# Optimization experiments

Measured on AMD Instinct MI355X. Metric: run time of the kernel, lower is better.

## Reference

```python
import jax, jax.numpy as jnp
import numpy as np

K = 0.001  # sigmoid temperature from DGCLoss init
EPS = 1e-8


def _off_diag(m):
    # [..., n, n] -> [..., n, n-1], removing the diagonal in row-major order
    n = m.shape[-1]
    lead = m.shape[:-2]
    flat = m.reshape(lead + (n * n,))[..., :-1]
    return flat.reshape(lead + (n - 1, n + 1))[..., 1:].reshape(lead + (n, n - 1))


def setup_inputs() -> dict:
    key = jax.random.key(0)
    k1, k2 = jax.random.split(key)
    ranking = jax.random.normal(k1, (384, 256), dtype=jnp.float32)
    gt = jax.random.randint(k2, (384,), 0, 6, dtype=jnp.int64)
    return {"ranking": ranking, "gt": gt}


def reference(ranking, gt):
    x = ranking
    N = x.shape[0]
    # cosine similarity matrix, mapped to [0, 1]
    xn = x / jnp.clip(jnp.linalg.norm(x, axis=1, keepdims=True), EPS, None)
    sm = (xn @ xn.T + 1.0) * 0.5                         # [N, N]
    rank = _off_diag(sm)                                 # [N, N-1]
    g = jnp.abs(gt[None, :] - gt[:, None]).astype(jnp.float32)  # [N, N]
    g = _off_diag(g)                                     # [N, N-1]
    M = N - 1
    # dij[n, i, j] = rank[n, j] - rank[n, i]
    dij = rank[:, None, :] - rank[:, :, None]            # [N, M, M]
    dij = _off_diag(dij)                                 # [N, M, M-1]
    # clamped sigmoid indicator
    indicator = 1.0 / (1.0 + jnp.exp(jnp.clip(-dij / K, -50.0, 50.0)))
    indicator = indicator.sum(-1) + 1.0                  # [N, M]
    relevance = jnp.exp2(jnp.clip(10.0 - g, 0.0, None)) - 1.0  # [N, M]
    dcg = (relevance / jnp.log2(indicator + 1.0)).sum(axis=1)  # [N]
    # ideal DCG from sorted relevance
    rel_sorted = jnp.sort(relevance, axis=-1)[:, ::-1]
    discount = jnp.log2(jnp.arange(M, dtype=jnp.float32) + 2.0)
    idcg = (rel_sorted / discount).sum(axis=-1)          # [N]
    valid = idcg != 0.0
    ndcg = jnp.where(valid, dcg / jnp.where(valid, idcg, 1.0), 0.0)
    cnt = valid.sum()
    mean_ndcg = ndcg.sum() / jnp.maximum(cnt, 1).astype(jnp.float32)
    return jnp.where(cnt == 0, jnp.float32(1.0), 1.0 - mean_ndcg)
```

## Files before the change

### kernel.cpp

```cpp
#include <hip/hip_runtime.h>


#define NN 384
#define DD 256
#define MM 383
#define HSCALE 721.3475204444817f
#define NBUCK  256
#define BSCALE 0.1767955801104972f
#define WWIN   16.0f

__global__ __launch_bounds__(256) void dgc_normT(const float* __restrict__ x,
                                                 float* __restrict__ XT,
                                                 float* __restrict__ XN,
                                                 float* __restrict__ out) {
    __shared__ float xs[16][260];
    __shared__ float invn[16];

    const int t  = threadIdx.x;
    const int r0 = blockIdx.x * 16;

    if (blockIdx.x == 0 && t == 0) out[0] = 1.0f;

    #pragma unroll
    for (int i = 0; i < 4; ++i) {
        int f = t + i * 256;
        int r = f >> 6, c4 = f & 63;
        float4 v = ((const float4*)(x + (size_t)(r0 + r) * DD))[c4];
        xs[r][c4 * 4 + 0] = v.x; xs[r][c4 * 4 + 1] = v.y;
        xs[r][c4 * 4 + 2] = v.z; xs[r][c4 * 4 + 3] = v.w;
    }
    __syncthreads();

    {
        const int r = t >> 4, sub = t & 15;
        float s = 0.0f;
        #pragma unroll
        for (int m = 0; m < 16; ++m) {
            float v = xs[r][sub * 16 + m];
            s = fmaf(v, v, s);
        }
        #pragma unroll
        for (int off = 8; off > 0; off >>= 1) s += __shfl_xor(s, off, 64);
        if (sub == 0) invn[r] = __builtin_amdgcn_rsqf(fmaxf(s, 1e-16f));
    }
    __syncthreads();

    {
        const int r  = t & 15;
        const int kk = t >> 4;
        const float inv = invn[r];
        #pragma unroll
        for (int i = 0; i < 16; ++i) {
            int k = i * 16 + kk;
            XT[(size_t)k * NN + r0 + r] = xs[r][k] * inv;
        }
    }
    {
        #pragma unroll
        for (int i = 0; i < 4; ++i) {
            int f = t + i * 256;
            int r = f >> 6, c4 = f & 63;
            const float inv = invn[r];
            float4 v;
            v.x = xs[r][c4 * 4 + 0] * inv; v.y = xs[r][c4 * 4 + 1] * inv;
            v.z = xs[r][c4 * 4 + 2] * inv; v.w = xs[r][c4 * 4 + 3] * inv;
            ((float4*)(XN + (size_t)(r0 + r) * DD))[c4] = v;
        }
    }
}

__global__ __launch_bounds__(384) void dgc_gram(const float* __restrict__ XN,
                                                const float* __restrict__ XT,
                                                float* __restrict__ S) {
    __shared__ __align__(16) float xs4[DD][4];

    const int t  = threadIdx.x;
    const int n0 = blockIdx.x * 4;

    if (t < 256) {
        int r = t >> 6, c4 = t & 63;
        float4 v = ((const float4*)(XN + (size_t)(n0 + r) * DD))[c4];
        xs4[c4 * 4 + 0][r] = v.x; xs4[c4 * 4 + 1][r] = v.y;
        xs4[c4 * 4 + 2][r] = v.z; xs4[c4 * 4 + 3][r] = v.w;
    }
    __syncthreads();

    const int j = t;
    float a0 = 0.f, a1 = 0.f, a2 = 0.f, a3 = 0.f;
    #pragma unroll 8
    for (int k = 0; k < DD; ++k) {
        float b = XT[(size_t)k * NN + j];
        float4 s = *(const float4*)xs4[k];
        a0 = fmaf(s.x, b, a0); a1 = fmaf(s.y, b, a1);
        a2 = fmaf(s.z, b, a2); a3 = fmaf(s.w, b, a3);
    }
    S[(size_t)(n0 + 0) * NN + j] = fmaf(a0, HSCALE, HSCALE);
    S[(size_t)(n0 + 1) * NN + j] = fmaf(a1, HSCALE, HSCALE);
    S[(size_t)(n0 + 2) * NN + j] = fmaf(a2, HSCALE, HSCALE);
    S[(size_t)(n0 + 3) * NN + j] = fmaf(a3, HSCALE, HSCALE);
}

__global__ __launch_bounds__(384) void dgc_body(const float* __restrict__ S,
                                                const int* __restrict__ gt,
                                                float* __restrict__ out) {
    __shared__ float vsort[NN];
    __shared__ int   sidx[NN];
    __shared__ int   hist[NBUCK];
    __shared__ int   pre[NBUCK + 1];
    __shared__ float sn_sh;
    __shared__ float redd[6], redi[6];
    __shared__ int   ghist[6], gcum[6];

    const int n    = blockIdx.x;
    const int t    = threadIdx.x;
    const int lane = t & 63;
    const int wave = t >> 6;

    const float vraw = S[(size_t)n * NN + t];
    if (t < NBUCK) hist[t] = 0;
    if (t < 6) ghist[t] = 0;
    if (t == n) sn_sh = vraw;
    __syncthreads();

    int b = (int)(vraw * BSCALE);
    b = b < 0 ? 0 : (b > NBUCK - 1 ? NBUCK - 1 : b);
    const int slot = atomicAdd(&hist[b], 1);
    __syncthreads();

    if (wave == 0) {
        const int s0 = hist[lane * 4 + 0], s1 = hist[lane * 4 + 1];
        const int s2 = hist[lane * 4 + 2], s3 = hist[lane * 4 + 3];
        const int sum = s0 + s1 + s2 + s3;
        int inc = sum;
        #pragma unroll
        for (int off = 1; off < 64; off <<= 1) {
            int u = __shfl_up(inc, off, 64);
            if (lane >= off) inc += u;
        }
        const int base = inc - sum;
        pre[lane * 4 + 0] = base;
        pre[lane * 4 + 1] = base + s0;
        pre[lane * 4 + 2] = base + s0 + s1;
        pre[lane * 4 + 3] = base + s0 + s1 + s2;
        if (lane == 63) pre[NBUCK] = inc;
    }
    __syncthreads();

    {
        const int pos = pre[b] + slot;
        vsort[pos] = vraw;
        sidx[pos]  = t;
    }
    __syncthreads();

    const float ri    = vsort[t];
    const int   iorig = sidx[t];
    const float sn    = sn_sh;

    int Blo = (int)((ri - WWIN) * BSCALE);
    int Bhi = (int)((ri + WWIN) * BSCALE);
    Blo = Blo < 0 ? 0 : (Blo > NBUCK - 1 ? NBUCK - 1 : Blo);
    Bhi = Bhi < 0 ? 0 : (Bhi > NBUCK - 1 ? NBUCK - 1 : Bhi);
    const int lo = pre[Blo];
    const int hi = pre[Bhi + 1];

    float p0 = 0.0f, p1 = 0.0f;
    int q = lo;
    for (; q + 2 <= hi; q += 2) {
        p0 += __builtin_amdgcn_rcpf(1.0f + __builtin_amdgcn_exp2f(ri - vsort[q]));
        p1 += __builtin_amdgcn_rcpf(1.0f + __builtin_amdgcn_exp2f(ri - vsort[q + 1]));
    }
    if (q < hi)
        p0 += __builtin_amdgcn_rcpf(1.0f + __builtin_amdgcn_exp2f(ri - vsort[q]));
    float sum_all = (float)(NN - hi) + p0 + p1;

    int bn = (int)(sn * BSCALE);
    bn = bn < 0 ? 0 : (bn > NBUCK - 1 ? NBUCK - 1 : bn);
    float cd = 0.0f;
    if (bn > Bhi)       cd = 1.0f;
    else if (bn >= Blo) cd = __builtin_amdgcn_rcpf(1.0f + __builtin_amdgcn_exp2f(ri - sn));
    const float ind = 0.5f + sum_all - cd;

    if (t < MM) {
        const int col = t + (t >= n ? 1 : 0);
        const int gd = gt[col] - gt[n];
        atomicAdd(&ghist[gd < 0 ? -gd : gd], 1);
    }
    __syncthreads();
    if (t == 0) {
        int s = 0;
        for (int g = 0; g < 6; ++g) { s += ghist[g]; gcum[g] = s; }
    }
    __syncthreads();

    float idcg_i = 0.0f;
    if (t < MM) {
        int p = t, g = 0;
        while (p >= gcum[g]) ++g;
        idcg_i = (float)((1 << (10 - g)) - 1) / __log2f((float)(p + 2));
    }

    float dcg_i = 0.0f;
    if (iorig != n) {
        const int gd = gt[iorig] - gt[n];
        const int gi = gd < 0 ? -gd : gd;
        dcg_i = (float)((1 << (10 - gi)) - 1) / __log2f(ind + 1.0f);
    }

    #pragma unroll
    for (int off = 32; off > 0; off >>= 1) {
        dcg_i  += __shfl_down(dcg_i,  off, 64);
        idcg_i += __shfl_down(idcg_i, off, 64);
    }
    if (lane == 0) { redd[wave] = dcg_i; redi[wave] = idcg_i; }
    __syncthreads();
    if (t == 0) {
        float d = 0.0f, id = 0.0f;
        for (int w = 0; w < 6; ++w) { d += redd[w]; id += redi[w]; }
        atomicAdd(out, -(d / id) * (1.0f / (float)NN));
    }
}

extern "C" void kernel_launch(void* const* d_in, const int* in_sizes, int n_in,
                              void* d_out, int out_size, void* d_ws, size_t ws_size,
                              hipStream_t stream) {
    const float* ranking = (const float*)d_in[0];
    const int*   gt      = (const int*)d_in[1];
    float*       out     = (float*)d_out;

    float* XT = (float*)d_ws;
    float* XN = XT + (size_t)DD * NN;
    float* S  = XN + (size_t)NN * DD;

    dgc_normT<<<24, 256, 0, stream>>>(ranking, XT, XN, out);
    dgc_gram<<<96, 384, 0, stream>>>(XN, XT, S);
    dgc_body<<<NN, 384, 0, stream>>>(S, gt, out);
}
```

Measured before the change: 82.88 us.

## Fuse Gram row computation into per-row NDCG kernel, drop S buffer

Removes the separate Gram kernel. Each per-row block now computes its own similarity row from the transposed normalized matrix and keeps it in shared memory, which drops one launch and the S round-trip through global memory. The cost is that each block reads all of XT (384x256 floats) alone, with no reuse across 4 rows as before. It also replaces the shared-memory atomic histogram of label gaps with wave ballots and popcounts, merging one sync stage, and uses the hardware log intrinsic.

```diff
diff --git a/kernel.cpp b/kernel.cpp
--- a/kernel.cpp
+++ b/kernel.cpp
@@ -69,62 +69,59 @@
     }
 }
 
-__global__ __launch_bounds__(384) void dgc_gram(const float* __restrict__ XN,
-                                                const float* __restrict__ XT,
-                                                float* __restrict__ S) {
-    __shared__ __align__(16) float xs4[DD][4];
-
-    const int t  = threadIdx.x;
-    const int n0 = blockIdx.x * 4;
-
-    if (t < 256) {
-        int r = t >> 6, c4 = t & 63;
-        float4 v = ((const float4*)(XN + (size_t)(n0 + r) * DD))[c4];
-        xs4[c4 * 4 + 0][r] = v.x; xs4[c4 * 4 + 1][r] = v.y;
-        xs4[c4 * 4 + 2][r] = v.z; xs4[c4 * 4 + 3][r] = v.w;
-    }
-    __syncthreads();
-
-    const int j = t;
-    float a0 = 0.f, a1 = 0.f, a2 = 0.f, a3 = 0.f;
-    #pragma unroll 8
-    for (int k = 0; k < DD; ++k) {
-        float b = XT[(size_t)k * NN + j];
-        float4 s = *(const float4*)xs4[k];
-        a0 = fmaf(s.x, b, a0); a1 = fmaf(s.y, b, a1);
-        a2 = fmaf(s.z, b, a2); a3 = fmaf(s.w, b, a3);
-    }
-    S[(size_t)(n0 + 0) * NN + j] = fmaf(a0, HSCALE, HSCALE);
-    S[(size_t)(n0 + 1) * NN + j] = fmaf(a1, HSCALE, HSCALE);
-    S[(size_t)(n0 + 2) * NN + j] = fmaf(a2, HSCALE, HSCALE);
-    S[(size_t)(n0 + 3) * NN + j] = fmaf(a3, HSCALE, HSCALE);
-}
-
-__global__ __launch_bounds__(384) void dgc_body(const float* __restrict__ S,
-                                                const int* __restrict__ gt,
-                                                float* __restrict__ out) {
+__global__ __launch_bounds__(384) void dgc_fused(const float* __restrict__ XT,
+                                                 const float* __restrict__ XN,
+                                                 const int* __restrict__ gt,
+                                                 float* __restrict__ out) {
+    __shared__ float xs[DD];
+    __shared__ float srow[NN];
     __shared__ float vsort[NN];
     __shared__ int   sidx[NN];
     __shared__ int   hist[NBUCK];
     __shared__ int   pre[NBUCK + 1];
-    __shared__ float sn_sh;
+    __shared__ int   wcnt[6][6];
+    __shared__ int   gcum[6];
     __shared__ float redd[6], redi[6];
-    __shared__ int   ghist[6], gcum[6];
 
     const int n    = blockIdx.x;
     const int t    = threadIdx.x;
     const int lane = t & 63;
     const int wave = t >> 6;
 
-    const float vraw = S[(size_t)n * NN + t];
+    if (t < DD / 4) ((float4*)xs)[t] = ((const float4*)(XN + (size_t)n * DD))[t];
     if (t < NBUCK) hist[t] = 0;
-    if (t < 6) ghist[t] = 0;
-    if (t == n) sn_sh = vraw;
-    __syncthreads();
+    __syncthreads();
+
+    {
+        const float* Xc = XT + t;
+        float d0 = 0.0f, d1 = 0.0f;
+        #pragma unroll 8
+        for (int k = 0; k < DD; k += 2) {
+            d0 = fmaf(xs[k],     Xc[(size_t)k * NN],       d0);
+            d1 = fmaf(xs[k + 1], Xc[(size_t)(k + 1) * NN], d1);
+        }
+        srow[t] = fmaf(d0 + d1, HSCALE, HSCALE);
+    }
+    __syncthreads();
+
+    const float vraw = srow[t];
+    const float sn   = srow[n];
 
     int b = (int)(vraw * BSCALE);
     b = b < 0 ? 0 : (b > NBUCK - 1 ? NBUCK - 1 : b);
     const int slot = atomicAdd(&hist[b], 1);
+
+    const bool validc = (t < MM);
+    int gi = 0;
+    if (validc) {
+        const int gd = gt[t + (t >= n ? 1 : 0)] - gt[n];
+        gi = gd < 0 ? -gd : gd;
+    }
+    #pragma unroll
+    for (int g = 0; g < 6; ++g) {
+        unsigned long long m = __ballot(validc && (gi == g));
+        if (lane == g) wcnt[wave][g] = __popcll(m);
+    }
     __syncthreads();
 
     if (wave == 0) {
@@ -144,6 +141,15 @@
         pre[lane * 4 + 3] = base + s0 + s1 + s2;
         if (lane == 63) pre[NBUCK] = inc;
     }
+    if (t == 0) {
+        int s = 0;
+        #pragma unroll
+        for (int g = 0; g < 6; ++g) {
+            s += wcnt[0][g] + wcnt[1][g] + wcnt[2][g]
+               + wcnt[3][g] + wcnt[4][g] + wcnt[5][g];
+            gcum[g] = s;
+        }
+    }
     __syncthreads();
 
     {
@@ -155,7 +161,6 @@
 
     const float ri    = vsort[t];
     const int   iorig = sidx[t];
-    const float sn    = sn_sh;
 
     int Blo = (int)((ri - WWIN) * BSCALE);
     int Bhi = (int)((ri + WWIN) * BSCALE);
@@ -181,30 +186,19 @@
     else if (bn >= Blo) cd = __builtin_amdgcn_rcpf(1.0f + __builtin_amdgcn_exp2f(ri - sn));
     const float ind = 0.5f + sum_all - cd;
 
-    if (t < MM) {
-        const int col = t + (t >= n ? 1 : 0);
-        const int gd = gt[col] - gt[n];
-        atomicAdd(&ghist[gd < 0 ? -gd : gd], 1);
-    }
-    __syncthreads();
-    if (t == 0) {
-        int s = 0;
-        for (int g = 0; g < 6; ++g) { s += ghist[g]; gcum[g] = s; }
-    }
-    __syncthreads();
-
     float idcg_i = 0.0f;
-    if (t < MM) {
-        int p = t, g = 0;
-        while (p >= gcum[g]) ++g;
-        idcg_i = (float)((1 << (10 - g)) - 1) / __log2f((float)(p + 2));
+    if (validc) {
+        const int p = t;
+        const int g = (p >= gcum[0]) + (p >= gcum[1]) + (p >= gcum[2])
+                    + (p >= gcum[3]) + (p >= gcum[4]);
+        idcg_i = (float)((1 << (10 - g)) - 1) / __builtin_amdgcn_logf((float)(p + 2));
     }
 
     float dcg_i = 0.0f;
     if (iorig != n) {
         const int gd = gt[iorig] - gt[n];
-        const int gi = gd < 0 ? -gd : gd;
-        dcg_i = (float)((1 << (10 - gi)) - 1) / __log2f(ind + 1.0f);
+        const int gg = gd < 0 ? -gd : gd;
+        dcg_i = (float)((1 << (10 - gg)) - 1) / __builtin_amdgcn_logf(ind + 1.0f);
     }
 
     #pragma unroll
@@ -216,6 +210,7 @@
     __syncthreads();
     if (t == 0) {
         float d = 0.0f, id = 0.0f;
+        #pragma unroll
         for (int w = 0; w < 6; ++w) { d += redd[w]; id += redi[w]; }
         atomicAdd(out, -(d / id) * (1.0f / (float)NN));
     }
@@ -230,9 +225,7 @@
 
     float* XT = (float*)d_ws;
     float* XN = XT + (size_t)DD * NN;
-    float* S  = XN + (size_t)NN * DD;
 
     dgc_normT<<<24, 256, 0, stream>>>(ranking, XT, XN, out);
-    dgc_gram<<<96, 384, 0, stream>>>(XN, XT, S);
-    dgc_body<<<NN, 384, 0, stream>>>(S, gt, out);
+    dgc_fused<<<NN, 384, 0, stream>>>(XT, XN, gt, out);
 }
```

New measurement: 74.52 us. 1.11x faster.
